# Performance work log

Measured on AMD Instinct MI355X. Metric: run time of the kernel, lower is better.

Reference implementation:

```python
import jax, jax.numpy as jnp
import numpy as np

N = 100000      # nodes
E = 1600000     # edges (before self-loops)
F_IN = 16       # num_node_features
HID = 16        # hid
HEADS = 4       # in_head == out_head
B = 64          # num graphs
G = 16          # num_global_features
NEG_SLOPE = 0.2


def gat_conv(x, src, dst, W, a_src, a_dst, b, concat):
    """PyG-style GATConv. x:[N,F], W:[F,H*C], a_src/a_dst:[H,C], b:[H*C] or [C]."""
    n = x.shape[0]
    H, C = a_src.shape
    h = (x @ W).reshape(n, H, C)                       # [N,H,C]
    alpha_s = (h * a_src).sum(-1)                      # [N,H]
    alpha_d = (h * a_dst).sum(-1)                      # [N,H]
    e = jax.nn.leaky_relu(alpha_s[src] + alpha_d[dst], NEG_SLOPE)  # [E',H]
    # segment softmax over destination nodes (stable; max is grad-free)
    m = jax.lax.stop_gradient(jax.ops.segment_max(e, dst, num_segments=n))
    ex = jnp.exp(e - m[dst])
    denom = jax.ops.segment_sum(ex, dst, num_segments=n)
    alpha = ex / (denom[dst] + 1e-16)                  # [E',H]
    out = jax.ops.segment_sum(h[src] * alpha[:, :, None], dst, num_segments=n)  # [N,H,C]
    out = out.reshape(n, H * C) if concat else out.mean(axis=1)
    return out + b


def setup_inputs() -> dict:
    key = jax.random.key(0)
    ks = jax.random.split(key, 24)
    s = 0.1
    inp = {
        "x": jax.random.normal(ks[0], (N, F_IN), jnp.float32),
        "stats": jax.random.normal(ks[1], (B, G), jnp.float32),
        # conv1: F_IN -> HID, heads=HEADS, concat=True
        "W1": jax.random.normal(ks[2], (F_IN, HEADS * HID), jnp.float32) * s,
        "a1s": jax.random.normal(ks[3], (HEADS, HID), jnp.float32) * s,
        "a1d": jax.random.normal(ks[4], (HEADS, HID), jnp.float32) * s,
        "b1": jnp.zeros((HEADS * HID,), jnp.float32),
        # conv2: HID*HEADS -> HID, heads=HEADS, concat=False
        "W2": jax.random.normal(ks[5], (HEADS * HID, HEADS * HID), jnp.float32) * s,
        "a2s": jax.random.normal(ks[6], (HEADS, HID), jnp.float32) * s,
        "a2d": jax.random.normal(ks[7], (HEADS, HID), jnp.float32) * s,
        "b2": jnp.zeros((HID,), jnp.float32),
        # conv3: HID -> HID, heads=HEADS, concat=False
        "W3": jax.random.normal(ks[8], (HID, HEADS * HID), jnp.float32) * s,
        "a3s": jax.random.normal(ks[9], (HEADS, HID), jnp.float32) * s,
        "a3d": jax.random.normal(ks[10], (HEADS, HID), jnp.float32) * s,
        "b3": jnp.zeros((HID,), jnp.float32),
        # MLP head
        "fw1": jax.random.normal(ks[11], (HID + G, 32), jnp.float32) * s,
        "fb1": jnp.zeros((32,), jnp.float32),
        "fw2": jax.random.normal(ks[12], (32, 16), jnp.float32) * s,
        "fb2": jnp.zeros((16,), jnp.float32),
        "fw3": jax.random.normal(ks[13], (16, 1), jnp.float32) * s,
        "fb3": jnp.zeros((1,), jnp.float32),
        "edge_index": jax.random.randint(ks[14], (2, E), 0, N, jnp.int64),
        "batch": jnp.sort(jax.random.randint(ks[15], (N,), 0, B, jnp.int64)),
    }
    return inp


def reference(x, stats, W1, a1s, a1d, b1, W2, a2s, a2d, b2, W3, a3s, a3d, b3,
              fw1, fb1, fw2, fb2, fw3, fb3, edge_index, batch):
    n = x.shape[0]
    loops = jnp.arange(n, dtype=edge_index.dtype)
    src = jnp.concatenate([edge_index[0], loops])  # add_self_loops=True (PyG default)
    dst = jnp.concatenate([edge_index[1], loops])
    h = jax.nn.elu(gat_conv(x, src, dst, W1, a1s, a1d, b1, True))
    h = jax.nn.elu(gat_conv(h, src, dst, W2, a2s, a2d, b2, False))
    h = gat_conv(h, src, dst, W3, a3s, a3d, b3, False)
    nb = stats.shape[0]
    pooled = jax.ops.segment_sum(h, batch, num_segments=nb)
    counts = jax.ops.segment_sum(jnp.ones((n,), h.dtype), batch, num_segments=nb)
    pooled = pooled / jnp.maximum(counts, 1.0)[:, None]   # global_mean_pool
    z = jnp.concatenate([pooled, stats], axis=1)
    z = jax.nn.relu(z @ fw1 + fb1)
    z = jax.nn.relu(z @ fw2 + fb2)
    return z @ fw3 + fb3
```

## Files before the change

kernel.cpp:

```cpp
#include <hip/hip_runtime.h>
#include <hip/hip_bf16.h>
#include <hip/hip_fp16.h>

#define NNODES 100000
#define NEDGES 1600000
#define NHEADS 4
#define NHID   16
#define NB     64
#define NG     16
#define POOL_BLOCKS 128
#define POOL_SLOTS (NB * NG + NB)

#define BKT_SHIFT 7
#define NPB 128
#define NBKT ((NNODES + NPB - 1) / NPB)
#define BCAP 4096
#define SCAT_BLOCKS 512
#define NL1_BLOCKS 2048

__device__ __forceinline__ float leaky02(float v) {
    return v > 0.0f ? v : 0.2f * v;
}

__device__ __forceinline__ float4 loadH4(const __half* p) {
    uint2 raw = *(const uint2*)p;
    __half2 a = *reinterpret_cast<const __half2*>(&raw.x);
    __half2 b = *reinterpret_cast<const __half2*>(&raw.y);
    float2 fa = __half22float2(a), fb = __half22float2(b);
    return make_float4(fa.x, fa.y, fb.x, fb.y);
}

__device__ __forceinline__ void storeH4(__half* p, float4 v) {
    __half2 a = __floats2half2_rn(v.x, v.y);
    __half2 b = __floats2half2_rn(v.z, v.w);
    uint2 raw;
    raw.x = *reinterpret_cast<unsigned*>(&a);
    raw.y = *reinterpret_cast<unsigned*>(&b);
    *(uint2*)p = raw;
}

template <int FIN>
__device__ __forceinline__ void nl_body_f32(const float* __restrict__ X,
                                            const float* __restrict__ W,
                                            const float* __restrict__ a_s,
                                            const float* __restrict__ a_d,
                                            __half* __restrict__ H,
                                            float* __restrict__ AS,
                                            float* __restrict__ AD, int n,
                                            int wave0, int nwaves, int lane) {
    int head = lane >> 4;
    float w[FIN];
#pragma unroll
    for (int k = 0; k < FIN; ++k) w[k] = W[k * 64 + lane];
    float asl = a_s[lane], adl = a_d[lane];

    for (int i = wave0; i < n; i += nwaves) {
        const float* __restrict__ xr = X + (size_t)i * FIN;
        float acc = 0.0f;
#pragma unroll
        for (int k = 0; k < FIN; ++k) acc += xr[k] * w[k];
        H[(size_t)i * 64 + lane] = __float2half_rn(acc);
        float s1 = acc * asl, s2 = acc * adl;
#pragma unroll
        for (int off = 1; off < 16; off <<= 1) {
            s1 += __shfl_xor(s1, off);
            s2 += __shfl_xor(s2, off);
        }
        if ((lane & 15) == 0) {
            AS[(size_t)i * 4 + head] = s1;
            AD[(size_t)i * 4 + head] = s2;
        }
    }
}

template <int FIN>
__global__ void node_linear3(const float* __restrict__ X,
                             const float* __restrict__ W,
                             const float* __restrict__ a_s,
                             const float* __restrict__ a_d,
                             __half* __restrict__ H,
                             float* __restrict__ AS,
                             float* __restrict__ AD, int n) {
    int lane = threadIdx.x & 63;
    int wave = __builtin_amdgcn_readfirstlane(
        (int)((blockIdx.x * blockDim.x + threadIdx.x) >> 6));
    int nwaves = (gridDim.x * blockDim.x) >> 6;
    nl_body_f32<FIN>(X, W, a_s, a_d, H, AS, AD, n, wave, nwaves, lane);
}

template <int FIN>
__global__ void node_linear3h(const unsigned* __restrict__ X,
                              const float* __restrict__ W,
                              const float* __restrict__ a_s,
                              const float* __restrict__ a_d,
                              __half* __restrict__ H,
                              float* __restrict__ AS,
                              float* __restrict__ AD, int n) {
    int lane = threadIdx.x & 63;
    int head = lane >> 4;
    int wave = __builtin_amdgcn_readfirstlane(
        (int)((blockIdx.x * blockDim.x + threadIdx.x) >> 6));
    int nwaves = (gridDim.x * blockDim.x) >> 6;

    float w[FIN];
#pragma unroll
    for (int k = 0; k < FIN; ++k) w[k] = W[k * 64 + lane];
    float asl = a_s[lane], adl = a_d[lane];

    for (int i = wave; i < n; i += nwaves) {
        const unsigned* __restrict__ xr = X + (size_t)i * (FIN / 2);
        float acc = 0.0f;
#pragma unroll
        for (int k = 0; k < FIN / 2; ++k) {
            unsigned u = xr[k];
            __half2 hh = *reinterpret_cast<const __half2*>(&u);
            float2 f = __half22float2(hh);
            acc += f.x * w[2 * k] + f.y * w[2 * k + 1];
        }
        H[(size_t)i * 64 + lane] = __float2half_rn(acc);
        float s1 = acc * asl, s2 = acc * adl;
#pragma unroll
        for (int off = 1; off < 16; off <<= 1) {
            s1 += __shfl_xor(s1, off);
            s2 += __shfl_xor(s2, off);
        }
        if ((lane & 15) == 0) {
            AS[(size_t)i * 4 + head] = s1;
            AD[(size_t)i * 4 + head] = s2;
        }
    }
}

__global__ void scatter_nl1(const int* __restrict__ src,
                            const int* __restrict__ dst,
                            int* __restrict__ bucketCnt,
                            unsigned int* __restrict__ pairs, int ne,
                            const float* __restrict__ X,
                            const float* __restrict__ W,
                            const float* __restrict__ a_s,
                            const float* __restrict__ a_d,
                            __half* __restrict__ H,
                            float* __restrict__ AS,
                            float* __restrict__ AD, int n) {
    __shared__ int hist[NBKT];
    __shared__ int base[NBKT];
    int tid = threadIdx.x;

    if (blockIdx.x >= SCAT_BLOCKS) {
        int lane = tid & 63;
        int wave = __builtin_amdgcn_readfirstlane(
            (int)(((blockIdx.x - SCAT_BLOCKS) * blockDim.x + tid) >> 6));
        int nwaves = (NL1_BLOCKS * 256) >> 6;
        nl_body_f32<16>(X, W, a_s, a_d, H, AS, AD, n, wave, nwaves, lane);
        return;
    }

    for (int i = tid; i < NBKT; i += 256) hist[i] = 0;
    __syncthreads();

    int chunk = (ne + SCAT_BLOCKS - 1) / SCAT_BLOCKS;
    int beg = blockIdx.x * chunk;
    int end = min(beg + chunk, ne);

    for (int e = beg + tid; e < end; e += 256)
        atomicAdd(&hist[dst[e] >> BKT_SHIFT], 1);
    __syncthreads();

    for (int i = tid; i < NBKT; i += 256) {
        int h = hist[i];
        base[i] = h ? atomicAdd(&bucketCnt[i], h) : 0;
        hist[i] = 0;
    }
    __syncthreads();

    for (int e = beg + tid; e < end; e += 256) {
        int d = dst[e];
        int bkt = d >> BKT_SHIFT;
        int r = base[bkt] + atomicAdd(&hist[bkt], 1);
        if (r < BCAP)
            pairs[(size_t)bkt * BCAP + r] =
                (unsigned)src[e] | ((unsigned)(d & (NPB - 1)) << 20);
    }
}

__global__ void bucket_scan(const int* __restrict__ bucketCnt,
                            int* __restrict__ bucketOff,
                            int* __restrict__ indptr, int n) {
    __shared__ int sd[1024];
    int t = threadIdx.x;
    int v = (t < NBKT) ? min(bucketCnt[t], BCAP) : 0;
    sd[t] = v;
    __syncthreads();
    for (int off = 1; off < 1024; off <<= 1) {
        int x = (t >= off) ? sd[t - off] : 0;
        __syncthreads();
        if (t >= off) sd[t] += x;
        __syncthreads();
    }
    if (t < NBKT) bucketOff[t] = sd[t] - v;
    if (t == NBKT - 1) {
        bucketOff[NBKT] = sd[t];
        indptr[n] = sd[t];
    }
}

__global__ void bucket_sort(const unsigned int* __restrict__ pairs,
                            const int* __restrict__ bucketCnt,
                            const int* __restrict__ bucketOff,
                            int* __restrict__ srcs,
                            int* __restrict__ indptr, int n) {
    __shared__ int hist[NPB];
    __shared__ int offl[NPB];
    __shared__ int cur[NPB];
    __shared__ int lsrc[BCAP];
    int bkt = blockIdx.x;
    int t = threadIdx.x;
    int cnt = min(bucketCnt[bkt], BCAP);
    int boff = bucketOff[bkt];
    if (t < NPB) hist[t] = 0;
    __syncthreads();

    const unsigned int* __restrict__ p = pairs + (size_t)bkt * BCAP;
    unsigned int v[BCAP / 256];
#pragma unroll
    for (int i = 0; i < BCAP / 256; ++i) {
        int e = i * 256 + t;
        v[i] = 0u;
        if (e < cnt) {
            v[i] = p[e];
            atomicAdd(&hist[v[i] >> 20], 1);
        }
    }
    __syncthreads();
    if (t < NPB) offl[t] = hist[t];
    __syncthreads();
    for (int off = 1; off < NPB; off <<= 1) {
        int x = 0;
        if (t < NPB && t >= off) x = offl[t - off];
        __syncthreads();
        if (t < NPB && t >= off) offl[t] += x;
        __syncthreads();
    }
    if (t < NPB) {
        int ex = offl[t] - hist[t];
        cur[t] = ex;
        int node = bkt * NPB + t;
        if (node < n) indptr[node] = boff + ex;
    }
    __syncthreads();
#pragma unroll
    for (int i = 0; i < BCAP / 256; ++i) {
        int e = i * 256 + t;
        if (e < cnt) {
            int r = atomicAdd(&cur[v[i] >> 20], 1);
            lsrc[r] = (int)(v[i] & 0xFFFFFu);
        }
    }
    __syncthreads();
    for (int e = t; e < cnt; e += 256) srcs[boff + e] = lsrc[e];
}

template <int MODE, typename TOUT>
__global__ void gat_pull3(const __half* __restrict__ H,
                          const float* __restrict__ AS,
                          const float* __restrict__ AD,
                          const int* __restrict__ indptr,
                          const int* __restrict__ srcs,
                          const float* __restrict__ bias,
                          TOUT* __restrict__ out, int n) {
    int lane = threadIdx.x & 63;
    int grp  = lane >> 4;
    int sl   = lane & 15;
    int head = sl >> 2;
    int wave = (blockIdx.x * blockDim.x + threadIdx.x) >> 6;
    int nwaves = (gridDim.x * blockDim.x) >> 6;

    for (int d0 = wave * 4; d0 < n; d0 += nwaves * 4) {
        int d = d0 + grp;
        if (d < n) {
            float ad  = AD[(size_t)d * 4 + head];
            float asd = AS[(size_t)d * 4 + head];
            float t0 = asd + ad;
            float wself = __expf(t0 > 0.f ? t0 : 0.2f * t0);
            float den = wself;
            float4 h4s = loadH4(H + (size_t)d * 64 + sl * 4);
            float4 acc = {wself * h4s.x, wself * h4s.y,
                          wself * h4s.z, wself * h4s.w};

            int beg = indptr[d], end = indptr[d + 1];
            for (int e0 = beg; e0 < end; e0 += 16) {
                int cnt = min(16, end - e0);
                int myS = (sl < cnt) ? srcs[e0 + sl] : 0;
                int j = 0;
                for (; j + 4 <= cnt; j += 4) {
                    int s[4]; float a[4]; float4 h4[4];
#pragma unroll
                    for (int q = 0; q < 4; ++q)
                        s[q] = __shfl(myS, (grp << 4) + j + q);
#pragma unroll
                    for (int q = 0; q < 4; ++q)
                        a[q] = AS[(size_t)s[q] * 4 + head];
#pragma unroll
                    for (int q = 0; q < 4; ++q)
                        h4[q] = loadH4(H + (size_t)s[q] * 64 + sl * 4);
#pragma unroll
                    for (int q = 0; q < 4; ++q) {
                        float t = a[q] + ad;
                        float w = __expf(t > 0.f ? t : 0.2f * t);
                        den += w;
                        acc.x += w * h4[q].x; acc.y += w * h4[q].y;
                        acc.z += w * h4[q].z; acc.w += w * h4[q].w;
                    }
                }
                for (; j < cnt; ++j) {
                    int s = __shfl(myS, (grp << 4) + j);
                    float t = AS[(size_t)s * 4 + head] + ad;
                    float w = __expf(t > 0.f ? t : 0.2f * t);
                    den += w;
                    float4 h4 = loadH4(H + (size_t)s * 64 + sl * 4);
                    acc.x += w * h4.x; acc.y += w * h4.y;
                    acc.z += w * h4.z; acc.w += w * h4.w;
                }
            }
            float inv = 1.0f / (den + 1e-16f);
            float4 v = {acc.x * inv, acc.y * inv, acc.z * inv, acc.w * inv};
            if (MODE == 0) {
                float4 b4 = *(const float4*)(bias + sl * 4);
                v.x += b4.x; v.y += b4.y; v.z += b4.z; v.w += b4.w;
                v.x = v.x > 0.f ? v.x : __expf(v.x) - 1.f;
                v.y = v.y > 0.f ? v.y : __expf(v.y) - 1.f;
                v.z = v.z > 0.f ? v.z : __expf(v.z) - 1.f;
                v.w = v.w > 0.f ? v.w : __expf(v.w) - 1.f;
                storeH4((__half*)out + (size_t)d * 64 + sl * 4, v);
            } else {
#pragma unroll
                for (int off = 4; off <= 8; off <<= 1) {
                    v.x += __shfl_xor(v.x, off);
                    v.y += __shfl_xor(v.y, off);
                    v.z += __shfl_xor(v.z, off);
                    v.w += __shfl_xor(v.w, off);
                }
                float4 b4 = *(const float4*)(bias + (sl & 3) * 4);
                v.x = 0.25f * v.x + b4.x; v.y = 0.25f * v.y + b4.y;
                v.z = 0.25f * v.z + b4.z; v.w = 0.25f * v.w + b4.w;
                if (MODE == 1) {
                    v.x = v.x > 0.f ? v.x : __expf(v.x) - 1.f;
                    v.y = v.y > 0.f ? v.y : __expf(v.y) - 1.f;
                    v.z = v.z > 0.f ? v.z : __expf(v.z) - 1.f;
                    v.w = v.w > 0.f ? v.w : __expf(v.w) - 1.f;
                }
                if (sl < 4)
                    *(float4*)((float*)out + (size_t)d * 16 + sl * 4) = v;
            }
        }
    }
}

__global__ void pool_stage1(const float* __restrict__ Hf,
                            const int* __restrict__ batch,
                            float* __restrict__ partials, int n) {
    __shared__ float lp[POOL_SLOTS];
    int tid = threadIdx.x;
    for (int i = tid; i < POOL_SLOTS; i += 256) lp[i] = 0.0f;
    __syncthreads();

    int chunk = (n + POOL_BLOCKS - 1) / POOL_BLOCKS;
    int start = blockIdx.x * chunk;
    int end = min(start + chunk, n);
    int c = tid & 15;
    for (int node = start + (tid >> 4); node < end; node += 16) {
        int b = batch[node];
        atomicAdd(&lp[b * 16 + c], Hf[(size_t)node * 16 + c]);
        if (c == 0) atomicAdd(&lp[NB * NG + b], 1.0f);
    }
    __syncthreads();
    float* outp = partials + (size_t)blockIdx.x * POOL_SLOTS;
    for (int i = tid; i < POOL_SLOTS; i += 256) outp[i] = lp[i];
}

__global__ void pool_stage2(const float* __restrict__ partials,
                            float* __restrict__ pooled_counts) {
    int idx = blockIdx.x * blockDim.x + threadIdx.x;
    if (idx >= POOL_SLOTS) return;
    float s = 0.0f;
    for (int j = 0; j < POOL_BLOCKS; ++j)
        s += partials[(size_t)j * POOL_SLOTS + idx];
    pooled_counts[idx] = s;
}

__global__ void mlp_head(const float* __restrict__ pooled_counts,
                         const float* __restrict__ stats,
                         const float* __restrict__ fw1, const float* __restrict__ fb1,
                         const float* __restrict__ fw2, const float* __restrict__ fb2,
                         const float* __restrict__ fw3, const float* __restrict__ fb3,
                         float* __restrict__ out) {
    int g = threadIdx.x;
    if (g >= NB) return;
    const float* pooled = pooled_counts;
    const float* counts = pooled_counts + NB * NG;
    float z[32];
    float inv = 1.0f / fmaxf(counts[g], 1.0f);
#pragma unroll
    for (int c = 0; c < 16; ++c) z[c] = pooled[g * 16 + c] * inv;
#pragma unroll
    for (int c = 0; c < 16; ++c) z[16 + c] = stats[g * 16 + c];

    float z1[32];
#pragma unroll
    for (int j = 0; j < 32; ++j) {
        float acc = fb1[j];
        for (int k = 0; k < 32; ++k) acc += z[k] * fw1[k * 32 + j];
        z1[j] = fmaxf(acc, 0.0f);
    }
    float z2[16];
#pragma unroll
    for (int j = 0; j < 16; ++j) {
        float acc = fb2[j];
        for (int k = 0; k < 32; ++k) acc += z1[k] * fw2[k * 16 + j];
        z2[j] = fmaxf(acc, 0.0f);
    }
    float acc = fb3[0];
#pragma unroll
    for (int k = 0; k < 16; ++k) acc += z2[k] * fw3[k];
    out[g] = acc;
}

extern "C" void kernel_launch(void* const* d_in, const int* in_sizes, int n_in,
                              void* d_out, int out_size, void* d_ws, size_t ws_size,
                              hipStream_t stream) {
    const float* x    = (const float*)d_in[0];
    const float* stats= (const float*)d_in[1];
    const float* W1   = (const float*)d_in[2];
    const float* a1s  = (const float*)d_in[3];
    const float* a1d  = (const float*)d_in[4];
    const float* b1   = (const float*)d_in[5];
    const float* W2   = (const float*)d_in[6];
    const float* a2s  = (const float*)d_in[7];
    const float* a2d  = (const float*)d_in[8];
    const float* b2   = (const float*)d_in[9];
    const float* W3   = (const float*)d_in[10];
    const float* a3s  = (const float*)d_in[11];
    const float* a3d  = (const float*)d_in[12];
    const float* b3   = (const float*)d_in[13];
    const float* fw1  = (const float*)d_in[14];
    const float* fb1  = (const float*)d_in[15];
    const float* fw2  = (const float*)d_in[16];
    const float* fb2  = (const float*)d_in[17];
    const float* fw3  = (const float*)d_in[18];
    const float* fb3  = (const float*)d_in[19];
    const int* ei     = (const int*)d_in[20];
    const int* batch  = (const int*)d_in[21];

    const int n = NNODES, ne = NEDGES;
    const int* srcI = ei;
    const int* dstI = ei + ne;

    float* ws = (float*)d_ws;
    __half* Hh  = (__half*)ws;
    float* B    = (float*)(Hh + (size_t)n * 64);
    __half* B16 = (__half*)B;
    float* C2   = B + (size_t)n * 64;
    float* AS   = C2 + (size_t)n * 16;
    float* AD   = AS + (size_t)n * 4;
    float* PC   = AD + (size_t)n * 4;
    float* PART = PC + POOL_SLOTS;
    int* bucketCnt = (int*)(PART + (size_t)POOL_BLOCKS * POOL_SLOTS);
    int* bucketOff = bucketCnt + NBKT;
    int* indptr    = bucketOff + NBKT + 1;
    int* srcs      = indptr + n + 1;
    unsigned int* pairs = (unsigned int*)B;

    const int TB = 256;
    const int nlBlocks   = 2048;
    const int pullBlocks = (n + 15) / 16;

    hipMemsetAsync(bucketCnt, 0, NBKT * sizeof(int), stream);
    scatter_nl1<<<SCAT_BLOCKS + NL1_BLOCKS, TB, 0, stream>>>(
        srcI, dstI, bucketCnt, pairs, ne,
        x, W1, a1s, a1d, Hh, AS, AD, n);
    bucket_scan<<<1, 1024, 0, stream>>>(bucketCnt, bucketOff, indptr, n);
    bucket_sort<<<NBKT, TB, 0, stream>>>(pairs, bucketCnt, bucketOff, srcs,
                                         indptr, n);

    gat_pull3<0, __half><<<pullBlocks, TB, 0, stream>>>(Hh, AS, AD, indptr, srcs, b1, B16, n);

    node_linear3h<64><<<nlBlocks, TB, 0, stream>>>((const unsigned*)B16, W2, a2s, a2d, Hh, AS, AD, n);
    gat_pull3<1, float><<<pullBlocks, TB, 0, stream>>>(Hh, AS, AD, indptr, srcs, b2, C2, n);

    node_linear3<16><<<nlBlocks, TB, 0, stream>>>(C2, W3, a3s, a3d, Hh, AS, AD, n);
    gat_pull3<2, float><<<pullBlocks, TB, 0, stream>>>(Hh, AS, AD, indptr, srcs, b3, B, n);

    pool_stage1<<<POOL_BLOCKS, TB, 0, stream>>>(B, batch, PART, n);
    pool_stage2<<<(POOL_SLOTS + TB - 1) / TB, TB, 0, stream>>>(PART, PC);
    mlp_head<<<1, 64, 0, stream>>>(PC, stats, fw1, fb1, fw2, fb2, fw3, fb3,
                                   (float*)d_out);
}
```

Baseline: 355.9 us.

## Fold bucket scan into bucket sort and batch edge loads in scatter

Result: faster. 337.3 us (-5.2%).

```diff
diff --git a/kernel.cpp b/kernel.cpp
--- a/kernel.cpp
+++ b/kernel.cpp
@@ -8,14 +8,14 @@
 #define NHID   16
 #define NB     64
 #define NG     16
-#define POOL_BLOCKS 128
+#define POOL_BLOCKS 256
 #define POOL_SLOTS (NB * NG + NB)
 
 #define BKT_SHIFT 7
 #define NPB 128
 #define NBKT ((NNODES + NPB - 1) / NPB)
 #define BCAP 4096
-#define SCAT_BLOCKS 512
+#define SCAT_BLOCKS 256
 #define NL1_BLOCKS 2048
 
 __device__ __forceinline__ float leaky02(float v) {
@@ -162,8 +162,17 @@
     int beg = blockIdx.x * chunk;
     int end = min(beg + chunk, ne);
 
-    for (int e = beg + tid; e < end; e += 256)
-        atomicAdd(&hist[dst[e] >> BKT_SHIFT], 1);
+    for (int e0 = beg; e0 < end; e0 += 1024) {
+        int d[4];
+#pragma unroll
+        for (int q = 0; q < 4; ++q) {
+            int e = e0 + q * 256 + tid;
+            d[q] = (e < end) ? dst[e] : -1;
+        }
+#pragma unroll
+        for (int q = 0; q < 4; ++q)
+            if (d[q] >= 0) atomicAdd(&hist[d[q] >> BKT_SHIFT], 1);
+    }
     __syncthreads();
 
     for (int i = tid; i < NBKT; i += 256) {
@@ -173,52 +182,55 @@
     }
     __syncthreads();
 
-    for (int e = beg + tid; e < end; e += 256) {
-        int d = dst[e];
-        int bkt = d >> BKT_SHIFT;
-        int r = base[bkt] + atomicAdd(&hist[bkt], 1);
-        if (r < BCAP)
-            pairs[(size_t)bkt * BCAP + r] =
-                (unsigned)src[e] | ((unsigned)(d & (NPB - 1)) << 20);
-    }
-}
-
-__global__ void bucket_scan(const int* __restrict__ bucketCnt,
-                            int* __restrict__ bucketOff,
-                            int* __restrict__ indptr, int n) {
-    __shared__ int sd[1024];
-    int t = threadIdx.x;
-    int v = (t < NBKT) ? min(bucketCnt[t], BCAP) : 0;
-    sd[t] = v;
-    __syncthreads();
-    for (int off = 1; off < 1024; off <<= 1) {
-        int x = (t >= off) ? sd[t - off] : 0;
-        __syncthreads();
-        if (t >= off) sd[t] += x;
-        __syncthreads();
-    }
-    if (t < NBKT) bucketOff[t] = sd[t] - v;
-    if (t == NBKT - 1) {
-        bucketOff[NBKT] = sd[t];
-        indptr[n] = sd[t];
+    for (int e0 = beg; e0 < end; e0 += 1024) {
+        int d[4], s[4];
+#pragma unroll
+        for (int q = 0; q < 4; ++q) {
+            int e = e0 + q * 256 + tid;
+            d[q] = (e < end) ? dst[e] : -1;
+            s[q] = (e < end) ? src[e] : 0;
+        }
+        int r[4], bkt[4];
+#pragma unroll
+        for (int q = 0; q < 4; ++q) {
+            if (d[q] >= 0) {
+                bkt[q] = d[q] >> BKT_SHIFT;
+                r[q] = base[bkt[q]] + atomicAdd(&hist[bkt[q]], 1);
+            }
+        }
+#pragma unroll
+        for (int q = 0; q < 4; ++q) {
+            if (d[q] >= 0 && r[q] < BCAP)
+                pairs[(size_t)bkt[q] * BCAP + r[q]] =
+                    (unsigned)s[q] | ((unsigned)(d[q] & (NPB - 1)) << 20);
+        }
     }
 }
 
 __global__ void bucket_sort(const unsigned int* __restrict__ pairs,
                             const int* __restrict__ bucketCnt,
-                            const int* __restrict__ bucketOff,
                             int* __restrict__ srcs,
                             int* __restrict__ indptr, int n) {
     __shared__ int hist[NPB];
     __shared__ int offl[NPB];
     __shared__ int cur[NPB];
+    __shared__ int red[256];
     __shared__ int lsrc[BCAP];
     int bkt = blockIdx.x;
     int t = threadIdx.x;
     int cnt = min(bucketCnt[bkt], BCAP);
-    int boff = bucketOff[bkt];
+
+    int partial = 0;
+    for (int j = t; j < bkt; j += 256) partial += min(bucketCnt[j], BCAP);
+    red[t] = partial;
     if (t < NPB) hist[t] = 0;
     __syncthreads();
+    for (int s = 128; s > 0; s >>= 1) {
+        if (t < s) red[t] += red[t + s];
+        __syncthreads();
+    }
+    int boff = red[0];
+    if (bkt == NBKT - 1 && t == 0) indptr[n] = boff + cnt;
 
     const unsigned int* __restrict__ p = pairs + (size_t)bkt * BCAP;
     unsigned int v[BCAP / 256];
@@ -465,8 +477,7 @@
     float* PC   = AD + (size_t)n * 4;
     float* PART = PC + POOL_SLOTS;
     int* bucketCnt = (int*)(PART + (size_t)POOL_BLOCKS * POOL_SLOTS);
-    int* bucketOff = bucketCnt + NBKT;
-    int* indptr    = bucketOff + NBKT + 1;
+    int* indptr    = bucketCnt + NBKT;
     int* srcs      = indptr + n + 1;
     unsigned int* pairs = (unsigned int*)B;
 
@@ -478,9 +489,7 @@
     scatter_nl1<<<SCAT_BLOCKS + NL1_BLOCKS, TB, 0, stream>>>(
         srcI, dstI, bucketCnt, pairs, ne,
         x, W1, a1s, a1d, Hh, AS, AD, n);
-    bucket_scan<<<1, 1024, 0, stream>>>(bucketCnt, bucketOff, indptr, n);
-    bucket_sort<<<NBKT, TB, 0, stream>>>(pairs, bucketCnt, bucketOff, srcs,
-                                         indptr, n);
+    bucket_sort<<<NBKT, TB, 0, stream>>>(pairs, bucketCnt, srcs, indptr, n);
 
     gat_pull3<0, __half><<<pullBlocks, TB, 0, stream>>>(Hh, AS, AD, indptr, srcs, b1, B16, n);
 
```
